# Performance work log

Measured on AMD Instinct MI355X. Metric: run time of the kernel, lower is better.

Reference implementation:

```python
import jax, jax.numpy as jnp
import numpy as np

B, N, M = 256, 4096, 16384
NUM_STEPS = 50
DT = 1.0
FP_THRES = 1e-3


def setup_inputs() -> dict:
    key = jax.random.key(0)
    k1, k2 = jax.random.split(key)
    inp = jax.random.normal(k1, (B, N, 1), dtype=jnp.float32)
    # xavier_normal for W [hidden, input]: std = sqrt(2/(fan_in+fan_out))
    std = np.sqrt(2.0 / (M + N)).astype(np.float32)
    W = jax.random.normal(k2, (M, N), dtype=jnp.float32) * std
    beta = jnp.float32(1.0)
    tau = jnp.float32(1.0)
    return {"input": inp, "W": W, "beta": beta, "tau": tau}


def reference(input, W, beta, tau):
    # Hopfield fixed-point iteration: v <- v + dt/tau * (W^T softmax(beta W v) - v)
    # input_mode='init' => state starts at input, no external current, no clamping.
    state0 = input  # [B, N, 1]
    done0 = jnp.array(False)

    def step(carry, _):
        state, done = carry
        h = jnp.einsum('mn,bno->bmo', W, state)            # [B, M, 1]
        f = jax.nn.softmax(beta * h, axis=-2)              # softmax over memory dim
        v_inst = jnp.einsum('mn,bmo->bno', W, f)           # [B, N, 1]
        new = state + (DT / tau) * (v_inst - state)
        # torch: update_magnitude = (prev_state - state).norm() (global Frobenius norm)
        upd = jnp.linalg.norm((new - state).reshape(-1))
        state_out = jnp.where(done, state, new)            # freeze once converged
        done = done | (upd <= FP_THRES)
        return (state_out, done), None

    (state, _), _ = jax.lax.scan(step, (state0, done0), None, length=NUM_STEPS)
    return state
```

## Files before the change

kernel.cpp:

```cpp
#include <hip/hip_runtime.h>
#include <hip/hip_cooperative_groups.h>

typedef __attribute__((ext_vector_type(8))) short short8;
typedef __attribute__((ext_vector_type(4))) float f32x4;
typedef __attribute__((ext_vector_type(2))) unsigned int u32x2;
typedef __attribute__((ext_vector_type(4))) unsigned int u32x4;

#define WS_ET   0u
#define WS_P2   8388608u
#define WS_ST   41943040u
#define WS_SB   46137344u
#define WS_CS   48234496u
#define WS_UG   48285696u
#define WS_CNT  48285952u
#define WS_WB   48298752u
#define WS_WBT  182516480u
#define WS_END  316734208u

#define WO_ET  0u
#define WO_P2  8388608u
#define WO_ST  25165824u
#define WO_SB  29360128u
#define WO_CS  31457280u
#define WO_UG  31508480u
#define WO_CNT 31508736u
#define WO_END 31534336u

static __device__ __forceinline__ unsigned short f2bf(float x) {
  union { float f; unsigned u; } v; v.f = x;
  unsigned r = v.u + 0x7FFFu + ((v.u >> 16) & 1u);
  return (unsigned short)(r >> 16);
}

static __device__ __forceinline__ void gl_lds16(const void* g, void* l) {
  __builtin_amdgcn_global_load_lds(
      (const __attribute__((address_space(1))) void*)g,
      (__attribute__((address_space(3))) void*)l, 16, 0, 0);
}

static __device__ __forceinline__ bool conv_before(const float* uG, int s) {
  bool d = false;
  for (int i = 0; i < s; ++i) d |= (uG[i] <= (-1.0f + 1.0e-6f));
  return d;
}

__global__ void sentinel_kernel(float* out, float v) { out[0] = v; }

__global__ void __launch_bounds__(256)
k0_setup(const float* __restrict__ inp, float* __restrict__ St,
         unsigned short* __restrict__ Sb, float* __restrict__ csG,
         float* __restrict__ uG, int* __restrict__ cnt)
{
  const int t = threadIdx.x, blk = blockIdx.x;
  if (blk == 0) {
    for (int i = t; i < 50 * 256; i += 256) csG[i] = 0.0f;
    if (t < 64) uG[t] = (t < 50) ? -1.0f : 0.0f;
  } else if (blk == 1) {
    for (int i = t; i < 50 * 64; i += 256) cnt[i] = 0;
  }
  #pragma unroll
  for (int i = 0; i < 8; ++i) {
    int idx = blk * 2048 + i * 256 + t;
    float v = inp[idx];
    Sb[idx] = f2bf(v);
    St[(idx & 4095) * 256 + (idx >> 12)] = v;
  }
}

__global__ void __launch_bounds__(256)
k0w_conv(const float* __restrict__ Wg, unsigned short* __restrict__ Wb,
         unsigned short* __restrict__ WbT)
{
  __shared__ unsigned short Tl[64][66];
  const int t = threadIdx.x;
  const int r = t >> 2, q = t & 3;
  for (int i = 0; i < 4; ++i) {
    const int ti = blockIdx.x * 4 + i;
    const int m0 = (ti >> 6) * 64;
    const int n0 = (ti & 63) * 64;
    const float* src = Wg + (size_t)(m0 + r) * 4096 + n0 + q * 16;
    unsigned short h[16] __attribute__((aligned(16)));
    #pragma unroll
    for (int v = 0; v < 4; ++v) {
      float4 f = *(const float4*)(src + v * 4);
      h[v*4+0] = f2bf(f.x); h[v*4+1] = f2bf(f.y);
      h[v*4+2] = f2bf(f.z); h[v*4+3] = f2bf(f.w);
    }
    unsigned short* wbp = Wb + (size_t)(m0 + r) * 4096 + n0 + q * 16;
    *(u32x4*)wbp       = *(const u32x4*)h;
    *(u32x4*)(wbp + 8) = *(const u32x4*)(h + 8);
    if (i) __syncthreads();
    #pragma unroll
    for (int k = 0; k < 16; ++k) Tl[r][q * 16 + k] = h[k];
    __syncthreads();
    unsigned short g[16] __attribute__((aligned(16)));
    const int nn = t >> 2;
    #pragma unroll
    for (int k = 0; k < 16; ++k) g[k] = Tl[q * 16 + k][nn];
    unsigned short* wtp = WbT + (size_t)(n0 + nn) * 16384 + m0 + q * 16;
    *(u32x4*)wtp       = *(const u32x4*)g;
    *(u32x4*)(wtp + 8) = *(const u32x4*)(g + 8);
  }
}

template<int ITERS, int AROWS, int BROWS>
static __device__ __forceinline__ void gemm_core(
    const unsigned short* __restrict__ Ag, const size_t lda, const int arow0,
    const unsigned short* __restrict__ Bg, const size_t ldb, const int brow0,
    const int kbase, unsigned short* smem, f32x4 (&acc)[AROWS/32][BROWS/32], const int t)
{
  constexpr int NR = AROWS / 32;
  constexpr int NC = BROWS / 32;
  const int lane = t & 63, wv = t >> 6;
  const int l15 = lane & 15, quad = lane >> 4;
  const int wr = wv >> 1, wc = wv & 1;
  const int xr = l15 & 7;
  unsigned short* As0 = smem;
  unsigned short* As1 = smem + AROWS * 64;
  unsigned short* Bs0 = smem + 2 * AROWS * 64;
  unsigned short* Bs1 = Bs0 + BROWS * 64;
  const int srow = wv * 8 + (lane >> 3);
  const int ks   = ((lane & 7) ^ (lane >> 3)) * 8;
  const unsigned short* gA = Ag + (size_t)(arow0 + srow) * lda + kbase + ks;
  const unsigned short* gB = Bg + (size_t)(brow0 + srow) * ldb + kbase + ks;
  const int sb = wv * 512;

#define STAGE_(itv, Ad, Bd)                                                       \
  { _Pragma("unroll") for (int j_ = 0; j_ < NR; ++j_)                             \
      gl_lds16(gA + (size_t)j_ * 32 * lda + (size_t)(itv) * 64, (Ad) + j_ * 2048 + sb); \
    _Pragma("unroll") for (int j_ = 0; j_ < NC; ++j_)                             \
      gl_lds16(gB + (size_t)j_ * 32 * ldb + (size_t)(itv) * 64, (Bd) + j_ * 2048 + sb); }

  STAGE_(0, As0, Bs0);
  __syncthreads();
  #pragma unroll 2
  for (int it = 0; it < ITERS; ++it) {
    unsigned short *Asc, *Bsc, *Asn, *Bsn;
    if (it & 1) { Asc = As1; Bsc = Bs1; Asn = As0; Bsn = Bs0; }
    else        { Asc = As0; Bsc = Bs0; Asn = As1; Bsn = Bs1; }
    if (it + 1 < ITERS) STAGE_(it + 1, Asn, Bsn);
    #pragma unroll
    for (int kk = 0; kk < 2; ++kk) {
      short8 af[NR], bq[NC];
      const int so = ((kk * 4 + quad) ^ xr) << 3;
      #pragma unroll
      for (int r = 0; r < NR; ++r)
        af[r] = *(const short8*)(Asc + (wr * (AROWS / 2) + r * 16 + l15) * 64 + so);
      #pragma unroll
      for (int c = 0; c < NC; ++c)
        bq[c] = *(const short8*)(Bsc + (wc * (BROWS / 2) + c * 16 + l15) * 64 + so);
      #pragma unroll
      for (int r = 0; r < NR; ++r)
        #pragma unroll
        for (int c = 0; c < NC; ++c)
          acc[r][c] = __builtin_amdgcn_mfma_f32_16x16x32_bf16(af[r], bq[c], acc[r][c], 0, 0, 0);
    }
    __syncthreads();
  }
#undef STAGE_
}

static __device__ __forceinline__ void gbar(int* ctr, int* gen, int nblk) {
  __syncthreads();
  if (threadIdx.x == 0) {
    __threadfence();
    int g = __hip_atomic_load(gen, __ATOMIC_RELAXED, __HIP_MEMORY_SCOPE_AGENT);
    int old = __hip_atomic_fetch_add(ctr, 1, __ATOMIC_RELAXED, __HIP_MEMORY_SCOPE_AGENT);
    if (old == nblk - 1) {
      __hip_atomic_store(ctr, 0, __ATOMIC_RELAXED, __HIP_MEMORY_SCOPE_AGENT);
      __hip_atomic_store(gen, g + 1, __ATOMIC_RELEASE, __HIP_MEMORY_SCOPE_AGENT);
    } else {
      while (__hip_atomic_load(gen, __ATOMIC_RELAXED, __HIP_MEMORY_SCOPE_AGENT) == g)
        __builtin_amdgcn_s_sleep(8);
    }
    __threadfence();
  }
  __syncthreads();
}

__global__ void __launch_bounds__(256, 2)
khop_pers(const unsigned short* __restrict__ Wb, const unsigned short* __restrict__ WbT,
          const float* __restrict__ betap, const float* __restrict__ taup,
          unsigned short* __restrict__ Et, float* __restrict__ P2,
          float* __restrict__ St, unsigned short* __restrict__ Sb,
          float* __restrict__ csG, float* __restrict__ uG,
          int* __restrict__ cnt, int* __restrict__ bar, float* __restrict__ out)
{
  __shared__ __align__(16) unsigned char smem_[65536];
  const int t = threadIdx.x, blk = blockIdx.x;
  const int w = ((blk & 7) << 6) | (blk >> 3);
  const int lane = t & 63, wv = t >> 6;
  const int l15 = lane & 15, quad = lane >> 4;
  const int wr = wv >> 1, wc = wv & 1;
  const float beta = betap[0];
  const float dtau = 1.0f / taup[0];
  int* bctr = bar;
  int* bgen = bar + 1;

  #pragma unroll 1
  for (int s = 0; s < 50; ++s) {
    {
      const int mt = w >> 1, bt = w & 1;
      const int m0 = mt * 64, b0 = bt * 128;
      f32x4 acc[2][4];
      #pragma unroll
      for (int r = 0; r < 2; ++r)
        #pragma unroll
        for (int c = 0; c < 4; ++c) { f32x4 z = {0.f,0.f,0.f,0.f}; acc[r][c] = z; }
      gemm_core<64, 64, 128>(Wb, 4096, m0, Sb, 4096, b0, 0, (unsigned short*)smem_, acc, t);
      #pragma unroll
      for (int c = 0; c < 4; ++c) {
        const int b = b0 + wc * 64 + c * 16 + l15;
        float cs = 0.0f;
        #pragma unroll
        for (int r = 0; r < 2; ++r) {
          unsigned short eb[4] __attribute__((aligned(8)));
          #pragma unroll
          for (int j = 0; j < 4; ++j) {
            float e = __expf(beta * acc[r][c][j]);
            cs += e;
            eb[j] = f2bf(e);
          }
          *(u32x2*)(Et + (size_t)b * 16384 + m0 + wr * 32 + r * 16 + quad * 4) = *(const u32x2*)eb;
        }
        cs += __shfl_xor(cs, 16, 64);
        cs += __shfl_xor(cs, 32, 64);
        if (quad == 0) atomicAdd(&csG[s * 256 + b], cs);
      }
    }
    gbar(bctr, bgen, 512);

    {
      const int kc = w >> 6, nt = (w & 63) >> 1, bt2 = w & 1;
      const int n0 = nt * 128, b0 = bt2 * 128;
      f32x4 acc[4][4];
      #pragma unroll
      for (int r = 0; r < 4; ++r)
        #pragma unroll
        for (int c = 0; c < 4; ++c) { f32x4 z = {0.f,0.f,0.f,0.f}; acc[r][c] = z; }
      gemm_core<32, 128, 128>(WbT, 16384, n0, Et, 16384, b0, kc * 2048, (unsigned short*)smem_, acc, t);
      float* Pd = P2 + (size_t)kc * 1048576;
      #pragma unroll
      for (int r = 0; r < 4; ++r) {
        const int n = n0 + wr * 64 + r * 16 + quad * 4;
        #pragma unroll
        for (int c = 0; c < 4; ++c) {
          const int b = b0 + wc * 64 + c * 16 + l15;
          #pragma unroll
          for (int j = 0; j < 4; ++j)
            Pd[(size_t)(n + j) * 256 + b] = acc[r][c][j];
        }
      }
      __syncthreads();
      if (t == 0) {
        __threadfence();
        int old = atomicAdd(&cnt[s * 64 + (nt * 2 + bt2)], 1);
        *(volatile int*)smem_ = (old == 7) ? 1 : 0;
      }
      __syncthreads();
      const bool last = (*(volatile int*)smem_ != 0);
      if (last) {
        if (t == 0) __threadfence();
        __syncthreads();
        float* T = (float*)smem_;
        float d2 = 0.0f;
        {
          const int bl = t & 127, th = t >> 7;
          const int bg = b0 + bl;
          const float inv = 1.0f / csG[s * 256 + bg];
          for (int i = 0; i < 64; ++i) {
            const int nl = i * 2 + th;
            const int n = n0 + nl;
            const float* pp = P2 + (size_t)n * 256 + bg;
            float sum = ((pp[0]       + pp[1048576]) + (pp[2097152] + pp[3145728]))
                      + ((pp[4194304] + pp[5242880]) + (pp[6291456] + pp[7340032]));
            float v = sum * inv;
            float old = St[n * 256 + bg];
            float nw = old + dtau * (v - old);
            float d = nw - old;
            d2 += d * d;
            St[n * 256 + bg] = nw;
            T[bl * 128 + (nl ^ (bl & 31))] = nw;
          }
        }
        __syncthreads();
        {
          const int nl = t & 127, th = t >> 7;
          #pragma unroll 4
          for (int p = 0; p < 64; ++p) {
            const int bl = p * 2 + th;
            out[(size_t)(b0 + bl) * 4096 + n0 + nl] = T[bl * 128 + (nl ^ (bl & 31))];
          }
        }
        {
          const int np = (t & 63) * 2, th = t >> 6;
          #pragma unroll 4
          for (int p = 0; p < 32; ++p) {
            const int bl = p * 4 + th;
            const int sw = bl & 31;
            float x0 = T[bl * 128 + (np ^ sw)];
            float x1 = T[bl * 128 + ((np + 1) ^ sw)];
            unsigned u = (unsigned)f2bf(x0) | ((unsigned)f2bf(x1) << 16);
            *(unsigned*)(Sb + (size_t)(b0 + bl) * 4096 + n0 + np) = u;
          }
        }
        #pragma unroll
        for (int o = 32; o > 0; o >>= 1) d2 += __shfl_down(d2, o, 64);
        __syncthreads();
        float* red = (float*)smem_;
        if (lane == 0) red[wv] = d2;
        __syncthreads();
        if (t == 0) atomicAdd(&uG[s], red[0] + red[1] + red[2] + red[3]);
      }
    }
    gbar(bctr, bgen, 512);
    const float u = __hip_atomic_load(&uG[s], __ATOMIC_RELAXED, __HIP_MEMORY_SCOPE_AGENT);
    if (u <= (-1.0f + 1.0e-6f)) break;
  }
}

__global__ void __launch_bounds__(256, 2)
k1_gemm1(const unsigned short* __restrict__ Wb, const float* __restrict__ betap,
         const unsigned short* __restrict__ Sb, unsigned short* __restrict__ Et,
         float* __restrict__ csG, const float* __restrict__ uG, int s)
{
  if (conv_before(uG, s)) return;
  __shared__ __align__(16) unsigned char smem_[65536];
  const int t = threadIdx.x;
  const int w = ((blockIdx.x & 7) << 5) | (blockIdx.x >> 3);
  const int mt = w >> 1, bt = w & 1;
  const int m0 = mt * 128, b0 = bt * 128;

  f32x4 acc[4][4];
  #pragma unroll
  for (int r = 0; r < 4; ++r)
    #pragma unroll
    for (int c = 0; c < 4; ++c) { f32x4 z = {0.f,0.f,0.f,0.f}; acc[r][c] = z; }

  gemm_core<64, 128, 128>(Wb, 4096, m0, Sb, 4096, b0, 0, (unsigned short*)smem_, acc, t);

  const float beta = betap[0];
  const int lane = t & 63, wv = t >> 6, l15 = lane & 15, quad = lane >> 4;
  const int wr = wv >> 1, wc = wv & 1;
  #pragma unroll
  for (int c = 0; c < 4; ++c) {
    const int b = b0 + wc * 64 + c * 16 + l15;
    float cs = 0.0f;
    #pragma unroll
    for (int r = 0; r < 4; ++r) {
      unsigned short eb[4] __attribute__((aligned(8)));
      #pragma unroll
      for (int j = 0; j < 4; ++j) {
        float e = __expf(beta * acc[r][c][j]);
        cs += e;
        eb[j] = f2bf(e);
      }
      *(u32x2*)(Et + (size_t)b * 16384 + m0 + wr * 64 + r * 16 + quad * 4) = *(const u32x2*)eb;
    }
    cs += __shfl_xor(cs, 16, 64);
    cs += __shfl_xor(cs, 32, 64);
    if (quad == 0) atomicAdd(&csG[s * 256 + b], cs);
  }
}

__global__ void __launch_bounds__(256, 2)
k2_gemm2(const unsigned short* __restrict__ WbT, const float* __restrict__ taup,
         const unsigned short* __restrict__ Et, float* __restrict__ P2,
         float* __restrict__ St, unsigned short* __restrict__ Sb,
         const float* __restrict__ csG, float* __restrict__ uG,
         int* __restrict__ cnt, float* __restrict__ out, int s)
{
  if (conv_before(uG, s)) return;
  __shared__ __align__(16) unsigned char smem_[65536];
  const int t = threadIdx.x;
  const int w = ((blockIdx.x & 7) << 6) | (blockIdx.x >> 3);
  const int kc = w >> 6, nt = (w & 63) >> 1, bt = w & 1;
  const int n0 = nt * 128, b0 = bt * 128;

  f32x4 acc[4][4];
  #pragma unroll
  for (int r = 0; r < 4; ++r)
    #pragma unroll
    for (int c = 0; c < 4; ++c) { f32x4 z = {0.f,0.f,0.f,0.f}; acc[r][c] = z; }

  gemm_core<32, 128, 128>(WbT, 16384, n0, Et, 16384, b0, kc * 2048, (unsigned short*)smem_, acc, t);

  const int lane = t & 63, wv = t >> 6, l15 = lane & 15, quad = lane >> 4;
  const int wr = wv >> 1, wc = wv & 1;
  float* Pd = P2 + (size_t)kc * 1048576;
  #pragma unroll
  for (int r = 0; r < 4; ++r) {
    const int n = n0 + wr * 64 + r * 16 + quad * 4;
    #pragma unroll
    for (int c = 0; c < 4; ++c) {
      const int b = b0 + wc * 64 + c * 16 + l15;
      #pragma unroll
      for (int j = 0; j < 4; ++j)
        Pd[(size_t)(n + j) * 256 + b] = acc[r][c][j];
    }
  }

  __syncthreads();
  if (t == 0) {
    __threadfence();
    int old = atomicAdd(&cnt[s * 64 + (nt * 2 + bt)], 1);
    *(volatile int*)smem_ = (old == 7) ? 1 : 0;
  }
  __syncthreads();
  const bool last = (*(volatile int*)smem_ != 0);
  if (!last) return;
  __threadfence();
  __syncthreads();

  const float dtau = 1.0f / taup[0];
  float* T = (float*)smem_;
  float d2 = 0.0f;
  {
    const int bl = t & 127, th = t >> 7;
    const int bg = b0 + bl;
    const float inv = 1.0f / csG[s * 256 + bg];
    for (int i = 0; i < 64; ++i) {
      const int nl = i * 2 + th;
      const int n = n0 + nl;
      const float* pp = P2 + (size_t)n * 256 + bg;
      float sum = ((pp[0]       + pp[1048576]) + (pp[2097152] + pp[3145728]))
                + ((pp[4194304] + pp[5242880]) + (pp[6291456] + pp[7340032]));
      float v = sum * inv;
      float old = St[n * 256 + bg];
      float nw = old + dtau * (v - old);
      float d = nw - old;
      d2 += d * d;
      St[n * 256 + bg] = nw;
      T[bl * 128 + (nl ^ (bl & 31))] = nw;
    }
  }
  __syncthreads();
  {
    const int nl = t & 127, th = t >> 7;
    #pragma unroll 4
    for (int p = 0; p < 64; ++p) {
      const int bl = p * 2 + th;
      out[(size_t)(b0 + bl) * 4096 + n0 + nl] = T[bl * 128 + (nl ^ (bl & 31))];
    }
  }
  {
    const int np = (t & 63) * 2, th = t >> 6;
    #pragma unroll 4
    for (int p = 0; p < 32; ++p) {
      const int bl = p * 4 + th;
      const int sw = bl & 31;
      float x0 = T[bl * 128 + (np ^ sw)];
      float x1 = T[bl * 128 + ((np + 1) ^ sw)];
      unsigned u = (unsigned)f2bf(x0) | ((unsigned)f2bf(x1) << 16);
      *(unsigned*)(Sb + (size_t)(b0 + bl) * 4096 + n0 + np) = u;
    }
  }
  #pragma unroll
  for (int o = 32; o > 0; o >>= 1) d2 += __shfl_down(d2, o, 64);
  __syncthreads();
  float* red = (float*)smem_;
  if (lane == 0) red[wv] = d2;
  __syncthreads();
  if (t == 0) atomicAdd(&uG[s], red[0] + red[1] + red[2] + red[3]);
}

__global__ void __launch_bounds__(256, 2)
k1_gemm1_o(const float* __restrict__ Wg, const float* __restrict__ betap,
           const unsigned short* __restrict__ Sb, unsigned short* __restrict__ Et,
           float* __restrict__ csG, const float* __restrict__ uG, int s)
{
  if (conv_before(uG, s)) return;
  __shared__ __align__(16) unsigned char smem[36864];
  const int t = threadIdx.x;
  const int lane = t & 63;
  const int wv = t >> 6;
  const int quad = lane >> 4;
  const int l15 = lane & 15;
  const float beta = betap[0];

  const int m0 = blockIdx.x * 32;
  unsigned short* As0 = (unsigned short*)(smem);
  unsigned short* As1 = (unsigned short*)(smem + 2048);
  unsigned short* Bs0 = (unsigned short*)(smem + 4096);
  unsigned short* Bs1 = (unsigned short*)(smem + 20480);
  const int ar = t >> 3;
  const int ac = (t & 7) * 4;
  const float* gA = Wg + (size_t)(m0 + ar) * 4096 + ac;
  const int brow = wv * 16 + (lane >> 2);
  const int bcol = (lane & 3) * 8;

  f32x4 acc[2][4];
  #pragma unroll
  for (int r = 0; r < 2; ++r)
    #pragma unroll
    for (int c = 0; c < 4; ++c) { f32x4 z = {0.f,0.f,0.f,0.f}; acc[r][c] = z; }

  float4 arA, arB;
#define LOADA1(itv, dst) { dst = *(const float4*)(gA + (itv) * 32); }
#define WRITEA1(Ad, src) { unsigned short p_[4] __attribute__((aligned(8)));        \
      p_[0]=f2bf((src).x); p_[1]=f2bf((src).y); p_[2]=f2bf((src).z); p_[3]=f2bf((src).w); \
      *(u32x2*)((Ad) + ar * 32 + ac) = *(const u32x2*)p_; }
#define STAGEB1(itv, Bd) { const int k0_ = (itv) * 32 + bcol;                       \
      _Pragma("unroll") for (int j_ = 0; j_ < 4; ++j_)                              \
        gl_lds16(Sb + (size_t)(j_ * 64 + brow) * 4096 + k0_, (Bd) + j_ * 2048 + wv * 512); }

  LOADA1(0, arA); STAGEB1(0, Bs0); WRITEA1(As0, arA); LOADA1(1, arB);
  __syncthreads();

  #pragma unroll 2
  for (int it = 0; it < 128; ++it) {
    unsigned short *Asc, *Bsc, *Asn, *Bsn;
    float4 *arC, *arN;
    if (it & 1) { Asc = As1; Bsc = Bs1; Asn = As0; Bsn = Bs0; arC = &arA; arN = &arB; }
    else        { Asc = As0; Bsc = Bs0; Asn = As1; Bsn = Bs1; arC = &arB; arN = &arA; }
    if (it + 2 < 128) LOADA1(it + 2, (*arN));
    if (it + 1 < 128) { STAGEB1(it + 1, Bsn); WRITEA1(Asn, (*arC)); }
    short8 af[2], bq[4];
    #pragma unroll
    for (int r = 0; r < 2; ++r) af[r] = *(const short8*)(Asc + (16 * r + l15) * 32 + quad * 8);
    #pragma unroll
    for (int c = 0; c < 4; ++c) bq[c] = *(const short8*)(Bsc + (64 * wv + 16 * c + l15) * 32 + quad * 8);
    #pragma unroll
    for (int r = 0; r < 2; ++r)
      #pragma unroll
      for (int c = 0; c < 4; ++c)
        acc[r][c] = __builtin_amdgcn_mfma_f32_16x16x32_bf16(af[r], bq[c], acc[r][c], 0, 0, 0);
    __syncthreads();
  }
#undef LOADA1
#undef WRITEA1
#undef STAGEB1
  #pragma unroll
  for (int c = 0; c < 4; ++c) {
    const int b = 64 * wv + 16 * c + l15;
    float cs = 0.0f;
    #pragma unroll
    for (int r = 0; r < 2; ++r) {
      unsigned short eb[4] __attribute__((aligned(8)));
      #pragma unroll
      for (int j = 0; j < 4; ++j) {
        float e = __expf(beta * acc[r][c][j]);
        cs += e;
        eb[j] = f2bf(e);
      }
      *(u32x2*)(Et + (size_t)b * 16384 + m0 + 16 * r + quad * 4) = *(const u32x2*)eb;
    }
    cs += __shfl_xor(cs, 16, 64);
    cs += __shfl_xor(cs, 32, 64);
    if (quad == 0) atomicAdd(&csG[s * 256 + b], cs);
  }
}

__global__ void __launch_bounds__(256, 2)
k2_gemm2_o(const float* __restrict__ Wg, const float* __restrict__ taup,
           const unsigned short* __restrict__ Et, float* __restrict__ P2,
           float* __restrict__ St, unsigned short* __restrict__ Sb,
           const float* __restrict__ csG, float* __restrict__ uG,
           int* __restrict__ cnt, float* __restrict__ out, int s)
{
  if (conv_before(uG, s)) return;
  __shared__ __align__(16) unsigned char smem[37888];
  __shared__ int lastF;
  const int t = threadIdx.x;
  const int lane = t & 63;
  const int wv = t >> 6;
  const int quad = lane >> 4;
  const int l15 = lane & 15;
  const int rt = blockIdx.x & 127;
  const int kc = blockIdx.x >> 7;
  const int n0 = rt * 32;
  const int mb = kc * 4096;

  unsigned short* As0 = (unsigned short*)(smem);
  unsigned short* As1 = (unsigned short*)(smem + 2560);
  unsigned short* Bs0 = (unsigned short*)(smem + 5120);
  unsigned short* Bs1 = (unsigned short*)(smem + 21504);
  const int mp = (t >> 4) * 2;
  const int ng = (t & 15) * 2;
  const int brow = wv * 16 + (lane >> 2);
  const int bcol = (lane & 3) * 8;

  f32x4 acc[2][4];
  #pragma unroll
  for (int r = 0; r < 2; ++r)
    #pragma unroll
    for (int c = 0; c < 4; ++c) { f32x4 z = {0.f,0.f,0.f,0.f}; acc[r][c] = z; }

  float2 aA0, aA1, aB0, aB1;
#define LOADA2(itv, d0, d1) { const float* g_ = Wg + (size_t)(mb + (itv) * 32 + mp) * 4096 + n0 + ng; \
      d0 = *(const float2*)g_; d1 = *(const float2*)(g_ + 4096); }
#define WRITEA2(Ad, d0, d1) {                                                       \
      unsigned x0_ = (unsigned)f2bf((d0).x) | ((unsigned)f2bf((d1).x) << 16);       \
      unsigned x1_ = (unsigned)f2bf((d0).y) | ((unsigned)f2bf((d1).y) << 16);       \
      *(unsigned*)((Ad) + ng * 40 + mp) = x0_;                                      \
      *(unsigned*)((Ad) + (ng + 1) * 40 + mp) = x1_; }
#define STAGEB2(itv, Bd) { const int k0_ = mb + (itv) * 32 + bcol;                  \
      _Pragma("unroll") for (int j_ = 0; j_ < 4; ++j_)                              \
        gl_lds16(Et + (size_t)(j_ * 64 + brow) * 16384 + k0_, (Bd) + j_ * 2048 + wv * 512); }

  LOADA2(0, aA0, aA1); STAGEB2(0, Bs0); WRITEA2(As0, aA0, aA1); LOADA2(1, aB0, aB1);
  __syncthreads();

  #pragma unroll 2
  for (int it = 0; it < 128; ++it) {
    unsigned short *Asc, *Bsc, *Asn, *Bsn;
    float2 *c0, *c1, *n0p, *n1p;
    if (it & 1) { Asc = As1; Bsc = Bs1; Asn = As0; Bsn = Bs0; c0 = &aA0; c1 = &aA1; n0p = &aB0; n1p = &aB1; }
    else        { Asc = As0; Bsc = Bs0; Asn = As1; Bsn = Bs1; c0 = &aB0; c1 = &aB1; n0p = &aA0; n1p = &aA1; }
    if (it + 2 < 128) LOADA2(it + 2, (*n0p), (*n1p));
    if (it + 1 < 128) { STAGEB2(it + 1, Bsn); WRITEA2(Asn, (*c0), (*c1)); }
    short8 af[2], bq[4];
    #pragma unroll
    for (int r = 0; r < 2; ++r) af[r] = *(const short8*)(Asc + (16 * r + l15) * 40 + quad * 8);
    #pragma unroll
    for (int c = 0; c < 4; ++c) bq[c] = *(const short8*)(Bsc + (64 * wv + 16 * c + l15) * 32 + quad * 8);
    #pragma unroll
    for (int r = 0; r < 2; ++r)
      #pragma unroll
      for (int c = 0; c < 4; ++c)
        acc[r][c] = __builtin_amdgcn_mfma_f32_16x16x32_bf16(af[r], bq[c], acc[r][c], 0, 0, 0);
    __syncthreads();
  }
#undef LOADA2
#undef WRITEA2
#undef STAGEB2
  float* Pd = P2 + (size_t)kc * 1048576;
  #pragma unroll
  for (int r = 0; r < 2; ++r)
    #pragma unroll
    for (int c = 0; c < 4; ++c) {
      const int b = 64 * wv + 16 * c + l15;
      #pragma unroll
      for (int j = 0; j < 4; ++j)
        Pd[(size_t)(n0 + 16 * r + quad * 4 + j) * 256 + b] = acc[r][c][j];
    }

  __syncthreads();
  if (t == 0) {
    __threadfence();
    int old = atomicAdd(&cnt[s * 128 + rt], 1);
    lastF = (old == 3);
  }
  __syncthreads();
  if (!lastF) return;
  __threadfence();

  const float dtau = 1.0f / taup[0];
  const float inv = 1.0f / csG[s * 256 + t];
  float* T = (float*)smem;
  float d2 = 0.0f;
  for (int i = 0; i < 32; ++i) {
    const int n = n0 + i;
    const float* pp = P2 + (size_t)n * 256 + t;
    float sum = pp[0] + pp[1048576] + pp[2097152] + pp[3145728];
    float v = sum * inv;
    float old = St[n * 256 + t];
    float nw = old + dtau * (v - old);
    float d = nw - old;
    d2 += d * d;
    St[n * 256 + t] = nw;
    T[t * 33 + i] = nw;
  }
  __syncthreads();
  #pragma unroll 4
  for (int p = 0; p < 32; ++p) {
    const int b = p * 8 + (t >> 5);
    const int nl = t & 31;
    out[(size_t)b * 4096 + n0 + nl] = T[b * 33 + nl];
  }
  #pragma unroll 4
  for (int p = 0; p < 16; ++p) {
    const int b = p * 16 + (t >> 4);
    const int np = (t & 15) * 2;
    unsigned u = (unsigned)f2bf(T[b * 33 + np]) | ((unsigned)f2bf(T[b * 33 + np + 1]) << 16);
    *(unsigned*)(Sb + (size_t)b * 4096 + n0 + np) = u;
  }
  #pragma unroll
  for (int o = 32; o > 0; o >>= 1) d2 += __shfl_down(d2, o, 64);
  __syncthreads();
  float* red = (float*)smem;
  if (lane == 0) red[wv] = d2;
  __syncthreads();
  if (t == 0) atomicAdd(&uG[s], red[0] + red[1] + red[2] + red[3]);
}

extern "C" void kernel_launch(void* const* d_in, const int* in_sizes, int n_in,
                              void* d_out, int out_size, void* d_ws, size_t ws_size,
                              hipStream_t stream) {
  const float* inp   = (const float*)d_in[0];
  const float* W     = (const float*)d_in[1];
  const float* betap = (const float*)d_in[2];
  const float* taup  = (const float*)d_in[3];
  float* out = (float*)d_out;
  char* ws = (char*)d_ws;

  if (ws_size >= (size_t)WS_END) {
    unsigned short* Et = (unsigned short*)(ws + WS_ET);
    float*          P2 = (float*)(ws + WS_P2);
    float*          St = (float*)(ws + WS_ST);
    unsigned short* Sb = (unsigned short*)(ws + WS_SB);
    float*          cs = (float*)(ws + WS_CS);
    float*          uG = (float*)(ws + WS_UG);
    int*            cn = (int*)(ws + WS_CNT);
    int*            br = (int*)(ws + WS_UG) + 56;
    unsigned short* Wb = (unsigned short*)(ws + WS_WB);
    unsigned short* Wt = (unsigned short*)(ws + WS_WBT);

    hipLaunchKernelGGL(k0_setup, dim3(512), dim3(256), 0, stream, inp, St, Sb, cs, uG, cn);
    hipLaunchKernelGGL(k0w_conv, dim3(4096), dim3(256), 0, stream, W, Wb, Wt);

    void* args[] = { &Wb, &Wt, &betap, &taup, &Et, &P2, &St, &Sb, &cs, &uG, &cn, &br, &out };
    hipError_t e = hipLaunchCooperativeKernel((const void*)khop_pers, dim3(512), dim3(256),
                                              (void**)args, 0, stream);
    if (e != hipSuccess) {
      for (int s = 0; s < 50; ++s) {
        hipLaunchKernelGGL(k1_gemm1, dim3(256), dim3(256), 0, stream, Wb, betap, Sb, Et, cs, uG, s);
        hipLaunchKernelGGL(k2_gemm2, dim3(512), dim3(256), 0, stream, Wt, taup, Et, P2, St, Sb, cs, uG, cn, out, s);
      }
    }
  } else if (ws_size >= (size_t)WO_END) {
    unsigned short* Et = (unsigned short*)(ws + WO_ET);
    float*          P2 = (float*)(ws + WO_P2);
    float*          St = (float*)(ws + WO_ST);
    unsigned short* Sb = (unsigned short*)(ws + WO_SB);
    float*          cs = (float*)(ws + WO_CS);
    float*          uG = (float*)(ws + WO_UG);
    int*            cn = (int*)(ws + WO_CNT);

    hipLaunchKernelGGL(k0_setup, dim3(512), dim3(256), 0, stream, inp, St, Sb, cs, uG, cn);
    for (int s = 0; s < 50; ++s) {
      hipLaunchKernelGGL(k1_gemm1_o, dim3(512), dim3(256), 0, stream, W, betap, Sb, Et, cs, uG, s);
      hipLaunchKernelGGL(k2_gemm2_o, dim3(512), dim3(256), 0, stream, W, taup, Et, P2, St, Sb, cs, uG, cn, out, s);
    }
  } else {
    hipLaunchKernelGGL(sentinel_kernel, dim3(1), dim3(1), 0, stream, out, 1.0e6f);
  }
}
```

Measured before the change: 1.311 ms.

## Replace last-block split-K reduction with grid-wide barrier and distributed state update

The split-K reduction and state update for the second GEMM were done by whichever block finished last per tile, serialising 128x128 epilogue work onto a few blocks. Now every block writes its partial result, all blocks meet at a grid barrier, and each of the 512 blocks reduces and updates 8 rows of N across all batch entries. The W conversion/transpose kernel also switches from 64x64 to 128x128 tiles with wider vector stores. This adds one extra grid barrier per step, while spreading the reduction evenly across the grid.

```diff
diff --git a/kernel.cpp b/kernel.cpp
--- a/kernel.cpp
+++ b/kernel.cpp
@@ -71,35 +71,34 @@
 k0w_conv(const float* __restrict__ Wg, unsigned short* __restrict__ Wb,
          unsigned short* __restrict__ WbT)
 {
-  __shared__ unsigned short Tl[64][66];
+  __shared__ __align__(16) unsigned short Ls[128][136];
   const int t = threadIdx.x;
-  const int r = t >> 2, q = t & 3;
-  for (int i = 0; i < 4; ++i) {
-    const int ti = blockIdx.x * 4 + i;
-    const int m0 = (ti >> 6) * 64;
-    const int n0 = (ti & 63) * 64;
-    const float* src = Wg + (size_t)(m0 + r) * 4096 + n0 + q * 16;
-    unsigned short h[16] __attribute__((aligned(16)));
-    #pragma unroll
-    for (int v = 0; v < 4; ++v) {
+  const int mb = blockIdx.x & 127, nb = blockIdx.x >> 7;
+  const int m0 = mb * 128, n0 = nb * 128;
+  {
+    const int r = t >> 1, c = (t & 1) * 64;
+    const float* src = Wg + (size_t)(m0 + r) * 4096 + n0 + c;
+    unsigned short h[64] __attribute__((aligned(16)));
+    #pragma unroll
+    for (int v = 0; v < 16; ++v) {
       float4 f = *(const float4*)(src + v * 4);
-      h[v*4+0] = f2bf(f.x); h[v*4+1] = f2bf(f.y);
-      h[v*4+2] = f2bf(f.z); h[v*4+3] = f2bf(f.w);
-    }
-    unsigned short* wbp = Wb + (size_t)(m0 + r) * 4096 + n0 + q * 16;
-    *(u32x4*)wbp       = *(const u32x4*)h;
-    *(u32x4*)(wbp + 8) = *(const u32x4*)(h + 8);
-    if (i) __syncthreads();
-    #pragma unroll
-    for (int k = 0; k < 16; ++k) Tl[r][q * 16 + k] = h[k];
-    __syncthreads();
-    unsigned short g[16] __attribute__((aligned(16)));
-    const int nn = t >> 2;
-    #pragma unroll
-    for (int k = 0; k < 16; ++k) g[k] = Tl[q * 16 + k][nn];
-    unsigned short* wtp = WbT + (size_t)(n0 + nn) * 16384 + m0 + q * 16;
-    *(u32x4*)wtp       = *(const u32x4*)g;
-    *(u32x4*)(wtp + 8) = *(const u32x4*)(g + 8);
+      h[v*4+0]=f2bf(f.x); h[v*4+1]=f2bf(f.y); h[v*4+2]=f2bf(f.z); h[v*4+3]=f2bf(f.w);
+    }
+    unsigned short* wbp = Wb + (size_t)(m0 + r) * 4096 + n0 + c;
+    #pragma unroll
+    for (int v = 0; v < 8; ++v) *(u32x4*)(wbp + v*8) = *(const u32x4*)(h + v*8);
+    #pragma unroll
+    for (int v = 0; v < 8; ++v) *(u32x4*)(&Ls[r][c + v*8]) = *(const u32x4*)(h + v*8);
+  }
+  __syncthreads();
+  {
+    const int n_l = t >> 1, mseg = (t & 1) * 64;
+    unsigned short g[64] __attribute__((aligned(16)));
+    #pragma unroll
+    for (int j = 0; j < 64; ++j) g[j] = Ls[mseg + j][n_l];
+    unsigned short* wtp = WbT + (size_t)(n0 + n_l) * 16384 + m0 + mseg;
+    #pragma unroll
+    for (int v = 0; v < 8; ++v) *(u32x4*)(wtp + v*8) = *(const u32x4*)(g + v*8);
   }
 }
 
@@ -251,67 +250,47 @@
             Pd[(size_t)(n + j) * 256 + b] = acc[r][c][j];
         }
       }
-      __syncthreads();
-      if (t == 0) {
-        __threadfence();
-        int old = atomicAdd(&cnt[s * 64 + (nt * 2 + bt2)], 1);
-        *(volatile int*)smem_ = (old == 7) ? 1 : 0;
+    }
+    gbar(bctr, bgen, 512);
+
+    {
+      const int n0 = blk * 8;
+      const float inv = 1.0f / csG[s * 256 + t];
+      float* T = (float*)smem_;
+      float d2 = 0.0f;
+      #pragma unroll
+      for (int i = 0; i < 8; ++i) {
+        const int n = n0 + i;
+        const float* pp = P2 + (size_t)n * 256 + t;
+        float sum = ((pp[0]       + pp[1048576]) + (pp[2097152] + pp[3145728]))
+                  + ((pp[4194304] + pp[5242880]) + (pp[6291456] + pp[7340032]));
+        float v = sum * inv;
+        float old = St[n * 256 + t];
+        float nw = old + dtau * (v - old);
+        float d = nw - old;
+        d2 += d * d;
+        St[n * 256 + t] = nw;
+        T[t * 9 + i] = nw;
       }
       __syncthreads();
-      const bool last = (*(volatile int*)smem_ != 0);
-      if (last) {
-        if (t == 0) __threadfence();
-        __syncthreads();
-        float* T = (float*)smem_;
-        float d2 = 0.0f;
-        {
-          const int bl = t & 127, th = t >> 7;
-          const int bg = b0 + bl;
-          const float inv = 1.0f / csG[s * 256 + bg];
-          for (int i = 0; i < 64; ++i) {
-            const int nl = i * 2 + th;
-            const int n = n0 + nl;
-            const float* pp = P2 + (size_t)n * 256 + bg;
-            float sum = ((pp[0]       + pp[1048576]) + (pp[2097152] + pp[3145728]))
-                      + ((pp[4194304] + pp[5242880]) + (pp[6291456] + pp[7340032]));
-            float v = sum * inv;
-            float old = St[n * 256 + bg];
-            float nw = old + dtau * (v - old);
-            float d = nw - old;
-            d2 += d * d;
-            St[n * 256 + bg] = nw;
-            T[bl * 128 + (nl ^ (bl & 31))] = nw;
-          }
-        }
-        __syncthreads();
-        {
-          const int nl = t & 127, th = t >> 7;
-          #pragma unroll 4
-          for (int p = 0; p < 64; ++p) {
-            const int bl = p * 2 + th;
-            out[(size_t)(b0 + bl) * 4096 + n0 + nl] = T[bl * 128 + (nl ^ (bl & 31))];
-          }
-        }
-        {
-          const int np = (t & 63) * 2, th = t >> 6;
-          #pragma unroll 4
-          for (int p = 0; p < 32; ++p) {
-            const int bl = p * 4 + th;
-            const int sw = bl & 31;
-            float x0 = T[bl * 128 + (np ^ sw)];
-            float x1 = T[bl * 128 + ((np + 1) ^ sw)];
-            unsigned u = (unsigned)f2bf(x0) | ((unsigned)f2bf(x1) << 16);
-            *(unsigned*)(Sb + (size_t)(b0 + bl) * 4096 + n0 + np) = u;
-          }
-        }
-        #pragma unroll
-        for (int o = 32; o > 0; o >>= 1) d2 += __shfl_down(d2, o, 64);
-        __syncthreads();
-        float* red = (float*)smem_;
-        if (lane == 0) red[wv] = d2;
-        __syncthreads();
-        if (t == 0) atomicAdd(&uG[s], red[0] + red[1] + red[2] + red[3]);
+      #pragma unroll
+      for (int p = 0; p < 8; ++p) {
+        const int b = p * 32 + (t >> 3);
+        out[(size_t)b * 4096 + n0 + (t & 7)] = T[b * 9 + (t & 7)];
       }
+      #pragma unroll
+      for (int p = 0; p < 4; ++p) {
+        const int b = p * 64 + (t >> 2);
+        const int np = (t & 3) * 2;
+        unsigned u = (unsigned)f2bf(T[b * 9 + np]) | ((unsigned)f2bf(T[b * 9 + np + 1]) << 16);
+        *(unsigned*)(Sb + (size_t)b * 4096 + n0 + np) = u;
+      }
+      #pragma unroll
+      for (int o = 32; o > 0; o >>= 1) d2 += __shfl_down(d2, o, 64);
+      float* red = (float*)(smem_ + 32768);
+      if (lane == 0) red[wv] = d2;
+      __syncthreads();
+      if (t == 0) atomicAdd(&uG[s], red[0] + red[1] + red[2] + red[3]);
     }
     gbar(bctr, bgen, 512);
     const float u = __hip_atomic_load(&uG[s], __ATOMIC_RELAXED, __HIP_MEMORY_SCOPE_AGENT);
```

Measured after the change: 1.538 ms. 17.3% more time.

## Use hierarchical grid barrier and larger-tile weight conversion transpose

Applied to the files above, without the earlier changes.

Replaces the flat 512-block atomic grid barrier with a two-level barrier: blocks first arrive on one of 8 padded group counters, and the last arrival in each group bumps a top-level counter. This cuts contention on a single atomic. The barrier state moves to its own zeroed workspace region. The W-to-bf16 conversion and transpose kernel is also restructured to handle one 128x128 tile per block, packing pairs of rows into 32-bit LDS words for wider transposed stores.

```diff
diff --git a/kernel.cpp b/kernel.cpp
--- a/kernel.cpp
+++ b/kernel.cpp
@@ -15,7 +15,8 @@
 #define WS_CNT  48285952u
 #define WS_WB   48298752u
 #define WS_WBT  182516480u
-#define WS_END  316734208u
+#define WS_BAR  316734208u
+#define WS_END  316738304u
 
 #define WO_ET  0u
 #define WO_P2  8388608u
@@ -49,7 +50,7 @@
 __global__ void __launch_bounds__(256)
 k0_setup(const float* __restrict__ inp, float* __restrict__ St,
          unsigned short* __restrict__ Sb, float* __restrict__ csG,
-         float* __restrict__ uG, int* __restrict__ cnt)
+         float* __restrict__ uG, int* __restrict__ cnt, int* __restrict__ barG)
 {
   const int t = threadIdx.x, blk = blockIdx.x;
   if (blk == 0) {
@@ -57,6 +58,8 @@
     if (t < 64) uG[t] = (t < 50) ? -1.0f : 0.0f;
   } else if (blk == 1) {
     for (int i = t; i < 50 * 64; i += 256) cnt[i] = 0;
+  } else if (blk == 2 && barG) {
+    for (int i = t; i < 1024; i += 256) barG[i] = 0;
   }
   #pragma unroll
   for (int i = 0; i < 8; ++i) {
@@ -71,35 +74,42 @@
 k0w_conv(const float* __restrict__ Wg, unsigned short* __restrict__ Wb,
          unsigned short* __restrict__ WbT)
 {
-  __shared__ unsigned short Tl[64][66];
+  __shared__ __align__(16) unsigned int Lt[128 * 65];
   const int t = threadIdx.x;
-  const int r = t >> 2, q = t & 3;
-  for (int i = 0; i < 4; ++i) {
-    const int ti = blockIdx.x * 4 + i;
-    const int m0 = (ti >> 6) * 64;
-    const int n0 = (ti & 63) * 64;
-    const float* src = Wg + (size_t)(m0 + r) * 4096 + n0 + q * 16;
-    unsigned short h[16] __attribute__((aligned(16)));
+  const int mb = blockIdx.x & 127, nb = blockIdx.x >> 7;
+  const int m0 = mb * 128, n0 = nb * 128;
+  {
+    const int mp = t & 63;
+    const int nseg = t >> 6;
+    const float* s0 = Wg + (size_t)(m0 + 2 * mp) * 4096 + n0 + nseg * 32;
+    const float* s1 = s0 + 4096;
+    unsigned short h0[32], h1[32];
+    #pragma unroll
+    for (int v = 0; v < 8; ++v) {
+      float4 f0 = *(const float4*)(s0 + v * 4);
+      float4 f1 = *(const float4*)(s1 + v * 4);
+      h0[v*4+0]=f2bf(f0.x); h0[v*4+1]=f2bf(f0.y); h0[v*4+2]=f2bf(f0.z); h0[v*4+3]=f2bf(f0.w);
+      h1[v*4+0]=f2bf(f1.x); h1[v*4+1]=f2bf(f1.y); h1[v*4+2]=f2bf(f1.z); h1[v*4+3]=f2bf(f1.w);
+    }
+    unsigned short* w0 = Wb + (size_t)(m0 + 2 * mp) * 4096 + n0 + nseg * 32;
     #pragma unroll
     for (int v = 0; v < 4; ++v) {
-      float4 f = *(const float4*)(src + v * 4);
-      h[v*4+0] = f2bf(f.x); h[v*4+1] = f2bf(f.y);
-      h[v*4+2] = f2bf(f.z); h[v*4+3] = f2bf(f.w);
-    }
-    unsigned short* wbp = Wb + (size_t)(m0 + r) * 4096 + n0 + q * 16;
-    *(u32x4*)wbp       = *(const u32x4*)h;
-    *(u32x4*)(wbp + 8) = *(const u32x4*)(h + 8);
-    if (i) __syncthreads();
-    #pragma unroll
-    for (int k = 0; k < 16; ++k) Tl[r][q * 16 + k] = h[k];
-    __syncthreads();
-    unsigned short g[16] __attribute__((aligned(16)));
-    const int nn = t >> 2;
-    #pragma unroll
-    for (int k = 0; k < 16; ++k) g[k] = Tl[q * 16 + k][nn];
-    unsigned short* wtp = WbT + (size_t)(n0 + nn) * 16384 + m0 + q * 16;
-    *(u32x4*)wtp       = *(const u32x4*)g;
-    *(u32x4*)(wtp + 8) = *(const u32x4*)(g + 8);
+      *(u32x4*)(w0 + v * 8)        = *(const u32x4*)(h0 + v * 8);
+      *(u32x4*)(w0 + 4096 + v * 8) = *(const u32x4*)(h1 + v * 8);
+    }
+    #pragma unroll
+    for (int j = 0; j < 32; ++j)
+      Lt[(nseg * 32 + j) * 65 + mp] = (unsigned)h0[j] | ((unsigned)h1[j] << 16);
+  }
+  __syncthreads();
+  {
+    const int n = t >> 1, mh = t & 1;
+    unsigned int w[32] __attribute__((aligned(16)));
+    #pragma unroll
+    for (int k = 0; k < 32; ++k) w[k] = Lt[n * 65 + mh * 32 + k];
+    unsigned short* dst = WbT + (size_t)(n0 + n) * 16384 + m0 + mh * 64;
+    #pragma unroll
+    for (int v = 0; v < 8; ++v) *(u32x4*)(dst + v * 8) = *(const u32x4*)(w + v * 4);
   }
 }
 
@@ -160,19 +170,26 @@
 #undef STAGE_
 }
 
-static __device__ __forceinline__ void gbar(int* ctr, int* gen, int nblk) {
+static __device__ __forceinline__ void gbar2(int* bar, int grp) {
   __syncthreads();
   if (threadIdx.x == 0) {
     __threadfence();
-    int g = __hip_atomic_load(gen, __ATOMIC_RELAXED, __HIP_MEMORY_SCOPE_AGENT);
-    int old = __hip_atomic_fetch_add(ctr, 1, __ATOMIC_RELAXED, __HIP_MEMORY_SCOPE_AGENT);
-    if (old == nblk - 1) {
-      __hip_atomic_store(ctr, 0, __ATOMIC_RELAXED, __HIP_MEMORY_SCOPE_AGENT);
-      __hip_atomic_store(gen, g + 1, __ATOMIC_RELEASE, __HIP_MEMORY_SCOPE_AGENT);
-    } else {
-      while (__hip_atomic_load(gen, __ATOMIC_RELAXED, __HIP_MEMORY_SCOPE_AGENT) == g)
-        __builtin_amdgcn_s_sleep(8);
-    }
+    int g = __hip_atomic_load(bar, __ATOMIC_RELAXED, __HIP_MEMORY_SCOPE_AGENT);
+    int old = __hip_atomic_fetch_add(&bar[32 + grp * 16], 1,
+                                     __ATOMIC_RELAXED, __HIP_MEMORY_SCOPE_AGENT);
+    if (old == 63) {
+      int o2 = __hip_atomic_fetch_add(&bar[16], 1,
+                                      __ATOMIC_RELAXED, __HIP_MEMORY_SCOPE_AGENT);
+      if (o2 == 7) {
+        __hip_atomic_store(&bar[16], 0, __ATOMIC_RELAXED, __HIP_MEMORY_SCOPE_AGENT);
+        #pragma unroll
+        for (int i = 0; i < 8; ++i)
+          __hip_atomic_store(&bar[32 + i * 16], 0, __ATOMIC_RELAXED, __HIP_MEMORY_SCOPE_AGENT);
+        __hip_atomic_store(bar, g + 1, __ATOMIC_RELEASE, __HIP_MEMORY_SCOPE_AGENT);
+      }
+    }
+    while (__hip_atomic_load(bar, __ATOMIC_RELAXED, __HIP_MEMORY_SCOPE_AGENT) == g)
+      __builtin_amdgcn_s_sleep(16);
     __threadfence();
   }
   __syncthreads();
@@ -189,15 +206,13 @@
   __shared__ __align__(16) unsigned char smem_[65536];
   const int t = threadIdx.x, blk = blockIdx.x;
   const int w = ((blk & 7) << 6) | (blk >> 3);
+  const int grp = blk & 7;
   const int lane = t & 63, wv = t >> 6;
   const int l15 = lane & 15, quad = lane >> 4;
   const int wr = wv >> 1, wc = wv & 1;
   const float beta = betap[0];
   const float dtau = 1.0f / taup[0];
-  int* bctr = bar;
-  int* bgen = bar + 1;
-
-  #pragma unroll 1
+
   for (int s = 0; s < 50; ++s) {
     {
       const int mt = w >> 1, bt = w & 1;
@@ -228,7 +243,7 @@
         if (quad == 0) atomicAdd(&csG[s * 256 + b], cs);
       }
     }
-    gbar(bctr, bgen, 512);
+    gbar2(bar, grp);
 
     {
       const int kc = w >> 6, nt = (w & 63) >> 1, bt2 = w & 1;
@@ -313,7 +328,7 @@
         if (t == 0) atomicAdd(&uG[s], red[0] + red[1] + red[2] + red[3]);
       }
     }
-    gbar(bctr, bgen, 512);
+    gbar2(bar, grp);
     const float u = __hip_atomic_load(&uG[s], __ATOMIC_RELAXED, __HIP_MEMORY_SCOPE_AGENT);
     if (u <= (-1.0f + 1.0e-6f)) break;
   }
@@ -702,11 +717,11 @@
     float*          cs = (float*)(ws + WS_CS);
     float*          uG = (float*)(ws + WS_UG);
     int*            cn = (int*)(ws + WS_CNT);
-    int*            br = (int*)(ws + WS_UG) + 56;
+    int*            br = (int*)(ws + WS_BAR);
     unsigned short* Wb = (unsigned short*)(ws + WS_WB);
     unsigned short* Wt = (unsigned short*)(ws + WS_WBT);
 
-    hipLaunchKernelGGL(k0_setup, dim3(512), dim3(256), 0, stream, inp, St, Sb, cs, uG, cn);
+    hipLaunchKernelGGL(k0_setup, dim3(512), dim3(256), 0, stream, inp, St, Sb, cs, uG, cn, br);
     hipLaunchKernelGGL(k0w_conv, dim3(4096), dim3(256), 0, stream, W, Wb, Wt);
 
     void* args[] = { &Wb, &Wt, &betap, &taup, &Et, &P2, &St, &Sb, &cs, &uG, &cn, &br, &out };
@@ -727,7 +742,7 @@
     float*          uG = (float*)(ws + WO_UG);
     int*            cn = (int*)(ws + WO_CNT);
 
-    hipLaunchKernelGGL(k0_setup, dim3(512), dim3(256), 0, stream, inp, St, Sb, cs, uG, cn);
+    hipLaunchKernelGGL(k0_setup, dim3(512), dim3(256), 0, stream, inp, St, Sb, cs, uG, cn, (int*)0);
     for (int s = 0; s < 50; ++s) {
       hipLaunchKernelGGL(k1_gemm1_o, dim3(512), dim3(256), 0, stream, W, betap, Sb, Et, cs, uG, s);
       hipLaunchKernelGGL(k2_gemm2_o, dim3(512), dim3(256), 0, stream, W, taup, Et, P2, St, Sb, cs, uG, cn, out, s);
```

Measured after the change: 1.251 ms. -4.6%, faster.
